# Kernel optimization log

Hardware: AMD Instinct MI355X
Metric: run time of the kernel (lower is better)

Reference implementation:

```python
import jax, jax.numpy as jnp
import numpy as np

B, S, E, H, DH, F = 4, 2048, 1024, 4, 256, 4096


def setup_inputs() -> dict:
    key = jax.random.key(0)
    ks = jax.random.split(key, 16)
    def w(k, shape):
        return jax.random.normal(k, shape, jnp.float32) * 0.02
    return {
        "inputs": jax.random.normal(ks[0], (B, S, E), jnp.float32),
        "context": jax.random.normal(ks[1], (B, S, E), jnp.float32),
        # self-attention (causal) per-head projections stacked over heads
        "Wk1": w(ks[2], (H, E, DH)), "bk1": jnp.zeros((H, DH), jnp.float32),
        "Wq1": w(ks[3], (H, E, DH)), "bq1": jnp.zeros((H, DH), jnp.float32),
        "Wv1": w(ks[4], (H, E, DH)), "bv1": jnp.zeros((H, DH), jnp.float32),
        "Wo1": w(ks[5], (E, E)), "bo1": jnp.zeros((E,), jnp.float32),
        # cross-attention (no mask)
        "Wk2": w(ks[6], (H, E, DH)), "bk2": jnp.zeros((H, DH), jnp.float32),
        "Wq2": w(ks[7], (H, E, DH)), "bq2": jnp.zeros((H, DH), jnp.float32),
        "Wv2": w(ks[8], (H, E, DH)), "bv2": jnp.zeros((H, DH), jnp.float32),
        "Wo2": w(ks[9], (E, E)), "bo2": jnp.zeros((E,), jnp.float32),
        "ln_g": jnp.ones((E,), jnp.float32), "ln_b": jnp.zeros((E,), jnp.float32),
        # FFN
        "W1": w(ks[10], (E, F)), "b1": jnp.zeros((F,), jnp.float32),
        "W2": w(ks[11], (F, E)), "b2": jnp.zeros((E,), jnp.float32),
    }


def _mha(kin, vin, qin, Wk, bk, Wq, bq, Wv, bv, Wo, bo, causal):
    # per-head Dense projections, batched over heads: [B,S,E] x [H,E,DH] -> [B,H,S,DH]
    K = jnp.einsum('bse,hed->bhsd', kin, Wk) + bk[None, :, None, :]
    Q = jnp.einsum('bse,hed->bhsd', qin, Wq) + bq[None, :, None, :]
    V = jnp.einsum('bse,hed->bhsd', vin, Wv) + bv[None, :, None, :]
    # NOTE: original divides by head_dim (K.get_shape()[2]), NOT sqrt(head_dim)
    scores = jnp.einsum('bhqd,bhkd->bhqk', Q, K) / K.shape[-1]
    if causal:
        sq, sk = scores.shape[-2], scores.shape[-1]
        mask = jnp.triu(jnp.full((sq, sk), -jnp.inf, scores.dtype), k=1)
        scores = scores + mask  # additive -inf strictly above the diagonal
    A = jax.nn.softmax(scores, axis=-1)
    # concat heads in order along the feature axis, then output Dense
    out = jnp.einsum('bhqk,bhkd->bqhd', A, V).reshape(qin.shape[0], qin.shape[1], -1)
    return out @ Wo + bo


def _ln(x, g, b):
    # keras LayerNormalization default epsilon = 1e-3
    m = x.mean(-1, keepdims=True)
    v = ((x - m) ** 2).mean(-1, keepdims=True)
    return (x - m) / jnp.sqrt(v + 1e-3) * g + b


def reference(inputs, context, Wk1, bk1, Wq1, bq1, Wv1, bv1, Wo1, bo1,
              Wk2, bk2, Wq2, bq2, Wv2, bv2, Wo2, bo2,
              ln_g, ln_b, W1, b1, W2, b2):
    # dropout layers are identity at inference
    a = _mha(inputs, inputs, inputs, Wk1, bk1, Wq1, bq1, Wv1, bv1, Wo1, bo1, True) + inputs
    a = _ln(a, ln_g, ln_b)
    # cross-attention: keys/values = context, queries = normalized self-attn output
    c = _mha(context, context, a, Wk2, bk2, Wq2, bq2, Wv2, bv2, Wo2, bo2, False) + a
    c = _ln(c, ln_g, ln_b)
    h = jax.nn.relu(c @ W1 + b1) @ W2 + b2 + c
    return jax.nn.relu(_ln(h, ln_g, ln_b))
```

## Files before the change

### kernel.cpp

```cpp
#include <hip/hip_runtime.h>

#define DEV __device__ __forceinline__

typedef unsigned short u16;
typedef __bf16 bf16x8 __attribute__((ext_vector_type(8)));
typedef bf16x8 __attribute__((may_alias)) bf16x8a;
typedef float f32x4 __attribute__((ext_vector_type(4)));
typedef float f32x16 __attribute__((ext_vector_type(16)));

constexpr int NB = 4, NS = 2048, NE = 1024, NH = 4, NDH = 256, NF = 4096;
constexpr int NR = NB * NS;

DEV u16 f2bf(float f) {
  unsigned u = __float_as_uint(f);
  u += 0x7fff + ((u >> 16) & 1);
  return (u16)(u >> 16);
}

DEV f32x4 mfma16(bf16x8 a, bf16x8 b, f32x4 c) {
  return __builtin_amdgcn_mfma_f32_16x16x32_bf16(a, b, c, 0, 0, 0);
}
DEV f32x16 mfma32(bf16x8 a, bf16x8 b, f32x16 c) {
  return __builtin_amdgcn_mfma_f32_32x32x16_bf16(a, b, c, 0, 0, 0);
}

DEV bf16x8 ldfrag(const u16* p) { return *(const bf16x8a*)p; }

DEV void gload_lds16(const void* g, void* l) {
  __builtin_amdgcn_global_load_lds(
      (const __attribute__((address_space(1))) void*)g,
      (__attribute__((address_space(3))) void*)l, 16, 0, 0);
}

DEV void blockbar() {
  asm volatile("" ::: "memory");
  __builtin_amdgcn_s_barrier();
  asm volatile("" ::: "memory");
}

DEV unsigned packbf(float a, float b) {
  union { __bf16 h[2]; unsigned u; } x;
  x.h[0] = (__bf16)a; x.h[1] = (__bf16)b;
  return x.u;
}

__global__ void cast_f32_bf16(const float* __restrict__ in, u16* __restrict__ out, int n4) {
  int i = blockIdx.x * 256 + threadIdx.x;
  if (i >= n4) return;
  float4 v = ((const float4*)in)[i];
  ushort4 o;
  o.x = f2bf(v.x); o.y = f2bf(v.y); o.z = f2bf(v.z); o.w = f2bf(v.w);
  ((ushort4*)out)[i] = o;
}

__global__ void transpose_cast(const float* __restrict__ in, u16* __restrict__ out, int R, int C) {
  __shared__ float t[32][33];
  size_t base = (size_t)blockIdx.z * R * C;
  int c0 = blockIdx.x * 32, r0 = blockIdx.y * 32;
  int x = threadIdx.x;
  for (int yy = threadIdx.y; yy < 32; yy += 8)
    t[yy][x] = in[base + (size_t)(r0 + yy) * C + c0 + x];
  __syncthreads();
  for (int yy = threadIdx.y; yy < 32; yy += 8)
    out[base + (size_t)(c0 + yy) * R + r0 + x] = f2bf(t[x][yy]);
}

__global__ void transpose_v(const u16* __restrict__ V, int vstride, u16* __restrict__ Vt) {
  __shared__ u16 t[32][34];
  int bh = blockIdx.z, b = bh >> 2, h = bh & (NH - 1);
  int s0 = blockIdx.x * 32, d0 = blockIdx.y * 32;
  int x = threadIdx.x;
  for (int yy = threadIdx.y; yy < 32; yy += 8)
    t[yy][x] = V[(size_t)(b * NS + s0 + yy) * vstride + h * NDH + d0 + x];
  __syncthreads();
  for (int yy = threadIdx.y; yy < 32; yy += 8)
    Vt[((size_t)bh * NDH + d0 + yy) * NS + s0 + x] = t[x][yy];
}

__global__ void copy_f32(const float* __restrict__ s, float* __restrict__ d, int n) {
  int i = blockIdx.x * 256 + threadIdx.x;
  if (i < n) d[i] = s[i];
}

template<int BN, int OUTF32, int RELU>
__global__ __launch_bounds__(512, 1)
void gemm8p(const u16* __restrict__ A, const u16* __restrict__ Bt,
            const float* __restrict__ bias, const float* __restrict__ res,
            float* __restrict__ outF, u16* __restrict__ outB,
            int M, int N, int K)
{
  constexpr int NFRAG = BN / 64;
  __shared__ __align__(16) u16 smem[32768 + 2 * BN * 64];

  int tid = threadIdx.x, w = tid >> 6, lane = tid & 63;
  int lr = lane & 15, lk = lane >> 4;
  int wm = w >> 2, wn = w & 3;

  int flat = blockIdx.y * gridDim.x + blockIdx.x;
  int cpx = (gridDim.x * gridDim.y) >> 3;
  int swz = (flat & 7) * cpx + (flat >> 3);
  int bx = swz % gridDim.x, by = swz / gridDim.x;
  int rowBlk = by * 256, colBlk = bx * BN;

  f32x4 acc[8][NFRAG];
#pragma unroll
  for (int f = 0; f < 8; f++)
#pragma unroll
    for (int n = 0; n < NFRAG; n++) acc[f][n] = (f32x4){0.f, 0.f, 0.f, 0.f};

  int srow = lane >> 3;
  int scol = ((lane & 7) ^ (srow & 7)) * 8;

  const u16* gA = A + (size_t)rowBlk * K;
  const u16* gB = Bt + (size_t)colBlk * K;

  auto stageA = [&](int t, int p, int h) {
#pragma unroll
    for (int j = 0; j < 2; j++) {
      int rbase = h * 128 + (w * 2 + j) * 8;
      gload_lds16(gA + (size_t)(rbase + srow) * K + t * 64 + scol,
                  &smem[(p * 256 + rbase) * 64]);
    }
  };
  auto stageB = [&](int t, int p, int h) {
#pragma unroll
    for (int j = 0; j < 2; j++) {
      int rbase = h * 128 + (w * 2 + j) * 8;
      gload_lds16(gB + (size_t)(rbase + srow) * K + t * 64 + scol,
                  &smem[32768 + (p * BN + rbase) * 64]);
    }
  };

  stageB(0, 0, 0);
  if (BN == 256) stageB(0, 0, 1);
  stageA(0, 0, 0);
  stageA(0, 0, 1);
  asm volatile("s_waitcnt vmcnt(0)" ::: "memory");
  blockbar();

  int NT = K >> 6;
  for (int t = 0; t < NT; t++) {
    int p = t & 1;
    bool pre = (t + 1 < NT);
    bf16x8 bf[NFRAG][2];
#pragma unroll
    for (int q = 0; q < 4; q++) {
      if (q == 0) {
#pragma unroll
        for (int n = 0; n < NFRAG; n++)
#pragma unroll
          for (int s = 0; s < 2; s++) {
            int rowB = wn * (BN >> 2) + n * 16 + lr;
            bf[n][s] = ldfrag(&smem[32768 + (p * BN + rowB) * 64 +
                                    (((s * 4 + lk) ^ (lr & 7)) * 8)]);
          }
      }
      bf16x8 af[2][2];
#pragma unroll
      for (int i = 0; i < 2; i++)
#pragma unroll
        for (int s = 0; s < 2; s++) {
          int rowA = wm * 128 + (q * 2 + i) * 16 + lr;
          af[i][s] = ldfrag(&smem[(p * 256 + rowA) * 64 +
                                  (((s * 4 + lk) ^ (lr & 7)) * 8)]);
        }
      if (pre) {
        if (BN == 256) {
          if (q == 0) { stageB(t + 1, p ^ 1, 0); stageB(t + 1, p ^ 1, 1); }
          else if (q == 1) stageA(t + 1, p ^ 1, 0);
          else if (q == 2) stageA(t + 1, p ^ 1, 1);
        } else {
          if (q == 0) stageB(t + 1, p ^ 1, 0);
          else if (q == 1) stageA(t + 1, p ^ 1, 0);
          else if (q == 2) stageA(t + 1, p ^ 1, 1);
        }
      }
      blockbar();
      asm volatile("s_waitcnt lgkmcnt(0)" ::: "memory");
      __builtin_amdgcn_s_setprio(1);
#pragma unroll
      for (int i = 0; i < 2; i++)
#pragma unroll
        for (int n = 0; n < NFRAG; n++)
#pragma unroll
          for (int s = 0; s < 2; s++)
            acc[q * 2 + i][n] = mfma16(af[i][s], bf[n][s], acc[q * 2 + i][n]);
      __builtin_amdgcn_s_setprio(0);
      if (q == 3) asm volatile("s_waitcnt vmcnt(0)" ::: "memory");
      blockbar();
    }
  }

  int orow0 = rowBlk + wm * 128;
  int ocol0 = colBlk + wn * (BN >> 2);
#pragma unroll
  for (int n = 0; n < NFRAG; n++) {
    int c = ocol0 + n * 16 + lr;
    float bv = bias[c];
#pragma unroll
    for (int f = 0; f < 8; f++) {
      int r0 = orow0 + f * 16 + lk * 4;
#pragma unroll
      for (int j = 0; j < 4; j++) {
        float v = acc[f][n][j] + bv;
        if (OUTF32) v += res[(size_t)(r0 + j) * N + c];
        if (RELU) v = fmaxf(v, 0.f);
        if (OUTF32) outF[(size_t)(r0 + j) * N + c] = v;
        else        outB[(size_t)(r0 + j) * N + c] = f2bf(v);
      }
    }
  }
}

template<int CAUSAL, int SPLIT>
__global__ __launch_bounds__(512, 2)
void attn8w(const u16* __restrict__ Qp, int qstride,
            const u16* __restrict__ Kp, int kstride,
            const u16* __restrict__ Vt, u16* __restrict__ O,
            float* __restrict__ Op, float* __restrict__ ml)
{
  __shared__ __align__(16) u16 smem[65536];

  int bidx = blockIdx.x;
  int bh, qt, kt0, kt1;
  if (SPLIT) {
    int qtIdx = bidx >> 5;
    qt = 15 - qtIdx;
    int sub = bidx & 31;
    int half = sub >> 4;
    bh = sub & 15;
    kt0 = half ? (qt + 1) : 0;
    kt1 = half ? (2 * qt + 2) : (qt + 1);
  } else {
    bh = bidx & 15;
    qt = CAUSAL ? (15 - (bidx >> 4)) : (bidx >> 4);
    kt0 = 0;
    kt1 = CAUSAL ? (2 * qt + 2) : (NS / 64);
  }
  int b = bh >> 2, h = bh & 3;
  int tid = threadIdx.x, w = tid >> 6, lane = tid & 63;
  int L = lane & 31, hi = lane >> 5;
  int g = w >> 1, ks = w & 1;

  int qbase = qt * 128 + g * 32;

  const u16* qrow = Qp + (size_t)(b * NS + qbase + L) * qstride + h * NDH;
  bf16x8 qf[16];
#pragma unroll
  for (int s = 0; s < 16; s++) qf[s] = ldfrag(qrow + s * 16 + hi * 8);

  f32x16 oacc[8];
#pragma unroll
  for (int db = 0; db < 8; db++) oacc[db] = (f32x16){};
  float m = -1e30f, l = 0.f;

  constexpr float SC = 1.0f / NDH;

  const u16* kbase = Kp + (size_t)(b * NS) * kstride + h * NDH;
  const u16* vbase = Vt + (size_t)bh * NDH * NS;

  auto stage = [&](int kt, int buf) {
#pragma unroll
    for (int ii = 0; ii < 4; ii++) {
      int gi = w * 4 + ii;
      int krow = 2 * gi + hi;
      int kcol = L ^ (krow & 31);
      gload_lds16(kbase + (size_t)(kt * 64 + krow) * kstride + kcol * 8,
                  &smem[buf * 16384 + gi * 512]);
      int vd = gi * 8 + (lane >> 3);
      int vg = (lane & 7) ^ (vd & 7);
      gload_lds16(vbase + (size_t)vd * NS + kt * 64 + vg * 8,
                  &smem[32768 + buf * 16384 + gi * 512]);
    }
  };

  stage(kt0, 0);
  asm volatile("" ::: "memory");

  for (int kt = kt0; kt < kt1; kt++) {
    int buf = (kt - kt0) & 1;
    const u16* bK = &smem[buf * 16384];
    const u16* bV = &smem[32768 + buf * 16384];
    if (kt + 1 < kt1) {
      stage(kt + 1, buf ^ 1);
      asm volatile("s_waitcnt vmcnt(8)" ::: "memory");
    } else {
      asm volatile("s_waitcnt vmcnt(0)" ::: "memory");
    }
    blockbar();

    int ksub0 = kt * 64 + ks * 32;
    bool skip = CAUSAL && (ksub0 > qbase + 31);
    if (!skip) {
      bool domask = CAUSAL && (ksub0 + 31 > qbase);
      __builtin_amdgcn_s_setprio(1);
      f32x16 sa = (f32x16){};
#pragma unroll
      for (int s = 0; s < 16; s++) {
        int row = ks * 32 + L;
        bf16x8 kf = ldfrag(&bK[row * 256 + (((2 * s + hi) ^ L) & 31) * 8]);
        sa = mfma32(kf, qf[s], sa);
      }
      __builtin_amdgcn_s_setprio(0);

      float p[16];
      float tmax = -1e30f;
#pragma unroll
      for (int r = 0; r < 16; r++) {
        float v = sa[r] * SC;
        if (domask) {
          int key = ksub0 + (r & 3) + 8 * (r >> 2) + 4 * hi;
          if (key > qbase + L) v = -1e30f;
        }
        p[r] = v;
        tmax = fmaxf(tmax, v);
      }
      tmax = fmaxf(tmax, __shfl_xor(tmax, 32));

      float mn = m;
      if (!__all(tmax - m <= 5.0f)) {
        mn = fmaxf(m, tmax);
        float rs = __expf(m - mn);
        m = mn;
        l *= rs;
#pragma unroll
        for (int db = 0; db < 8; db++)
#pragma unroll
          for (int r = 0; r < 16; r++) oacc[db][r] *= rs;
      }
      float psum = 0.f;
#pragma unroll
      for (int r = 0; r < 16; r++) {
        p[r] = __expf(p[r] - mn);
        psum += p[r];
      }
      psum += __shfl_xor(psum, 32);
      l += psum;

      unsigned pk01 = packbf(p[0], p[1]),  pk23 = packbf(p[2], p[3]);
      unsigned pk45 = packbf(p[4], p[5]),  pk67 = packbf(p[6], p[7]);
      unsigned pk89 = packbf(p[8], p[9]),  pkab = packbf(p[10], p[11]);
      unsigned pkcd = packbf(p[12], p[13]), pkef = packbf(p[14], p[15]);
      unsigned s45 = (unsigned)__shfl_xor((int)pk45, 32);
      unsigned s67 = (unsigned)__shfl_xor((int)pk67, 32);
      unsigned s01 = (unsigned)__shfl_xor((int)pk01, 32);
      unsigned s23 = (unsigned)__shfl_xor((int)pk23, 32);
      unsigned scd = (unsigned)__shfl_xor((int)pkcd, 32);
      unsigned sef = (unsigned)__shfl_xor((int)pkef, 32);
      unsigned s89 = (unsigned)__shfl_xor((int)pk89, 32);
      unsigned sab = (unsigned)__shfl_xor((int)pkab, 32);
      union { unsigned u[4]; bf16x8 v; } fb0, fb1;
      fb0.u[0] = hi ? s45 : pk01;
      fb0.u[1] = hi ? s67 : pk23;
      fb0.u[2] = hi ? pk45 : s01;
      fb0.u[3] = hi ? pk67 : s23;
      fb1.u[0] = hi ? scd : pk89;
      fb1.u[1] = hi ? sef : pkab;
      fb1.u[2] = hi ? pkcd : s89;
      fb1.u[3] = hi ? pkef : sab;
      bf16x8 pb0 = fb0.v, pb1 = fb1.v;

      __builtin_amdgcn_s_setprio(1);
#pragma unroll
      for (int db = 0; db < 8; db++) {
        int vd = db * 32 + L;
        bf16x8 vf0 = ldfrag(&bV[vd * 64 + (((ks * 4 + hi) ^ (vd & 7)) & 7) * 8]);
        bf16x8 vf1 = ldfrag(&bV[vd * 64 + (((ks * 4 + 2 + hi) ^ (vd & 7)) & 7) * 8]);
        oacc[db] = mfma32(vf0, pb0, oacc[db]);
        oacc[db] = mfma32(vf1, pb1, oacc[db]);
      }
      __builtin_amdgcn_s_setprio(0);
    }
    blockbar();
  }

  float* fsm = (float*)smem;
  blockbar();
  if (hi == 0) { fsm[w * 64 + L * 2] = m; fsm[w * 64 + L * 2 + 1] = l; }
  asm volatile("s_waitcnt lgkmcnt(0)" ::: "memory");
  blockbar();
  float mb = fsm[(w ^ 1) * 64 + L * 2];
  float lb = fsm[(w ^ 1) * 64 + L * 2 + 1];
  float M = fmaxf(m, mb);
  float eo = __expf(m - M);
  float lt = l * eo + lb * __expf(mb - M);
  asm volatile("s_waitcnt lgkmcnt(0)" ::: "memory");
  blockbar();
  float* reg = fsm + g * 8192;
  if (w & 1) {
#pragma unroll
    for (int db = 0; db < 8; db++)
#pragma unroll
      for (int r = 0; r < 16; r++) {
        int d = db * 32 + (r & 3) + 8 * (r >> 2) + 4 * hi;
        reg[d * 32 + L] = oacc[db][r] * eo;
      }
  }
  asm volatile("s_waitcnt lgkmcnt(0)" ::: "memory");
  blockbar();
  if (!(w & 1)) {
    if (SPLIT) {
      float* OpB = Op + (size_t)bidx * 32768 + (size_t)(g * 32 + L) * 256;
      if (hi == 0) {
        ml[((size_t)bidx * 128 + g * 32 + L) * 2]     = M;
        ml[((size_t)bidx * 128 + g * 32 + L) * 2 + 1] = lt;
      }
#pragma unroll
      for (int db = 0; db < 8; db++) {
#pragma unroll
        for (int rq = 0; rq < 4; rq++) {
          int d0 = db * 32 + rq * 8 + hi * 4;
          float4 v;
          v.x = oacc[db][rq * 4 + 0] * eo + reg[(d0 + 0) * 32 + L];
          v.y = oacc[db][rq * 4 + 1] * eo + reg[(d0 + 1) * 32 + L];
          v.z = oacc[db][rq * 4 + 2] * eo + reg[(d0 + 2) * 32 + L];
          v.w = oacc[db][rq * 4 + 3] * eo + reg[(d0 + 3) * 32 + L];
          *(float4*)(OpB + d0) = v;
        }
      }
    } else {
      float inv = 1.f / lt;
      size_t orow = (size_t)(b * NS + qbase + L) * NE + h * NDH;
#pragma unroll
      for (int db = 0; db < 8; db++) {
#pragma unroll
        for (int rq = 0; rq < 4; rq++) {
          int d0 = db * 32 + rq * 8 + hi * 4;
          float a0 = (oacc[db][rq * 4 + 0] * eo + reg[(d0 + 0) * 32 + L]) * inv;
          float a1 = (oacc[db][rq * 4 + 1] * eo + reg[(d0 + 1) * 32 + L]) * inv;
          float a2 = (oacc[db][rq * 4 + 2] * eo + reg[(d0 + 2) * 32 + L]) * inv;
          float a3 = (oacc[db][rq * 4 + 3] * eo + reg[(d0 + 3) * 32 + L]) * inv;
          uint2 wv;
          wv.x = packbf(a0, a1);
          wv.y = packbf(a2, a3);
          *(uint2*)&O[orow + d0] = wv;
        }
      }
    }
  }
}

__global__ __launch_bounds__(256)
void merge_attn(const float* __restrict__ Op, const float* __restrict__ ml,
                u16* __restrict__ O)
{
  int blk = blockIdx.x;
  int qt = blk >> 4, bh = blk & 15;
  int b = bh >> 2, h = bh & 3;
  int p0 = (15 - qt) * 32 + bh;
  int p1 = p0 + 16;
  int tid = threadIdx.x;
  int row = tid >> 1;
  int dbase = (tid & 1) * 128;

  float m0 = ml[((size_t)p0 * 128 + row) * 2];
  float l0 = ml[((size_t)p0 * 128 + row) * 2 + 1];
  float m1 = ml[((size_t)p1 * 128 + row) * 2];
  float l1 = ml[((size_t)p1 * 128 + row) * 2 + 1];
  float M = fmaxf(m0, m1);
  float e0 = __expf(m0 - M), e1 = __expf(m1 - M);
  float inv = 1.f / (l0 * e0 + l1 * e1);
  const float* O0 = Op + ((size_t)p0 * 128 + row) * 256 + dbase;
  const float* O1 = Op + ((size_t)p1 * 128 + row) * 256 + dbase;
  u16* dst = O + (size_t)(b * NS + qt * 128 + row) * NE + h * NDH + dbase;
#pragma unroll
  for (int d = 0; d < 128; d += 4) {
    float4 a = *(const float4*)(O0 + d);
    float4 c = *(const float4*)(O1 + d);
    uint2 wv;
    wv.x = packbf((a.x * e0 + c.x * e1) * inv, (a.y * e0 + c.y * e1) * inv);
    wv.y = packbf((a.z * e0 + c.z * e1) * inv, (a.w * e0 + c.w * e1) * inv);
    *(uint2*)(dst + d) = wv;
  }
}

template<int RELU, int WBF>
__global__ __launch_bounds__(256)
void ln_kernel(const float* __restrict__ x, const float* __restrict__ g,
               const float* __restrict__ bb, float* __restrict__ outF,
               u16* __restrict__ outB)
{
  int row = blockIdx.x, tid = threadIdx.x;
  float4 v = ((const float4*)(x + (size_t)row * NE))[tid];
  float s = v.x + v.y + v.z + v.w;
  float s2 = v.x * v.x + v.y * v.y + v.z * v.z + v.w * v.w;
#pragma unroll
  for (int off = 32; off; off >>= 1) {
    s += __shfl_xor(s, off);
    s2 += __shfl_xor(s2, off);
  }
  __shared__ float red[8];
  int wid = tid >> 6, lane = tid & 63;
  if (lane == 0) { red[wid] = s; red[4 + wid] = s2; }
  __syncthreads();
  s = red[0] + red[1] + red[2] + red[3];
  s2 = red[4] + red[5] + red[6] + red[7];
  float mean = s * (1.f / NE);
  float var = s2 * (1.f / NE) - mean * mean;
  float rstd = rsqrtf(var + 1e-3f);
  float4 gg = ((const float4*)g)[tid];
  float4 bv = ((const float4*)bb)[tid];
  float4 o;
  o.x = (v.x - mean) * rstd * gg.x + bv.x;
  o.y = (v.y - mean) * rstd * gg.y + bv.y;
  o.z = (v.z - mean) * rstd * gg.z + bv.z;
  o.w = (v.w - mean) * rstd * gg.w + bv.w;
  if (RELU) {
    o.x = fmaxf(o.x, 0.f); o.y = fmaxf(o.y, 0.f);
    o.z = fmaxf(o.z, 0.f); o.w = fmaxf(o.w, 0.f);
  }
  ((float4*)(outF + (size_t)row * NE))[tid] = o;
  if (WBF) {
    ushort4 ob;
    ob.x = f2bf(o.x); ob.y = f2bf(o.y); ob.z = f2bf(o.z); ob.w = f2bf(o.w);
    ((ushort4*)(outB + (size_t)row * NE))[tid] = ob;
  }
}

constexpr size_t OFF_X    = 0;
constexpr size_t OFF_W    = OFF_X + 16777216;
constexpr size_t OFF_BIAS = OFF_W + 33554432;
constexpr size_t OFF_QKV  = OFF_BIAS + 32768;
constexpr size_t OFF_VT   = OFF_QKV + 50331648;
constexpr size_t OFF_T0   = OFF_VT + 16777216;
constexpr size_t OFF_A    = OFF_T0 + 33554432;
constexpr size_t OFF_ABF  = OFF_A + 33554432;

extern "C" void kernel_launch(void* const* d_in, const int* in_sizes, int n_in,
                              void* d_out, int out_size, void* d_ws, size_t ws_size,
                              hipStream_t stream) {
  (void)in_sizes; (void)n_in; (void)out_size; (void)ws_size;
  const float* inp = (const float*)d_in[0];
  const float* ctx = (const float*)d_in[1];
  const float* Wk1 = (const float*)d_in[2];  const float* bk1 = (const float*)d_in[3];
  const float* Wq1 = (const float*)d_in[4];  const float* bq1 = (const float*)d_in[5];
  const float* Wv1 = (const float*)d_in[6];  const float* bv1 = (const float*)d_in[7];
  const float* Wo1 = (const float*)d_in[8];  const float* bo1 = (const float*)d_in[9];
  const float* Wk2 = (const float*)d_in[10]; const float* bk2 = (const float*)d_in[11];
  const float* Wq2 = (const float*)d_in[12]; const float* bq2 = (const float*)d_in[13];
  const float* Wv2 = (const float*)d_in[14]; const float* bv2 = (const float*)d_in[15];
  const float* Wo2 = (const float*)d_in[16]; const float* bo2 = (const float*)d_in[17];
  const float* lng = (const float*)d_in[18]; const float* lnb = (const float*)d_in[19];
  const float* W1  = (const float*)d_in[20]; const float* b1  = (const float*)d_in[21];
  const float* W2  = (const float*)d_in[22]; const float* b2  = (const float*)d_in[23];
  float* out = (float*)d_out;
  char* ws = (char*)d_ws;

  u16* XBF    = (u16*)(ws + OFF_X);
  u16* WQKV1T = (u16*)(ws + OFF_W);
  u16* WKV2T  = WQKV1T + 3072 * 1024;
  u16* WQ2T   = WKV2T + 2048 * 1024;
  u16* WO1T   = WQ2T + 1024 * 1024;
  u16* WO2T   = WO1T + 1024 * 1024;
  u16* W1T    = WO2T + 1024 * 1024;
  u16* W2T    = W1T + 4096 * 1024;
  float* BQKV1 = (float*)(ws + OFF_BIAS);
  float* BKV2  = BQKV1 + 3072;
  u16* QKV  = (u16*)(ws + OFF_QKV);
  u16* Q2   = QKV + 8192 * 2048;
  u16* VT   = (u16*)(ws + OFF_VT);
  u16* MID  = QKV;
  float* T0 = (float*)(ws + OFF_T0);
  float* OpBuf = T0;
  float* Af = (float*)(ws + OFF_A);
  u16* ABF  = (u16*)(ws + OFF_ABF);
  float* MlBuf = (float*)(ws + OFF_ABF);
  u16* Obuf = XBF;

  dim3 tb(32, 8);

  cast_f32_bf16<<<8192, 256, 0, stream>>>(inp, XBF, NR * NE / 4);
  transpose_cast<<<dim3(8, 32, 4), tb, 0, stream>>>(Wk1, WQKV1T,               NE, NDH);
  transpose_cast<<<dim3(8, 32, 4), tb, 0, stream>>>(Wq1, WQKV1T + 1024 * 1024, NE, NDH);
  transpose_cast<<<dim3(8, 32, 4), tb, 0, stream>>>(Wv1, WQKV1T + 2048 * 1024, NE, NDH);
  transpose_cast<<<dim3(32, 32, 1), tb, 0, stream>>>(Wo1, WO1T, NE, NE);
  transpose_cast<<<dim3(8, 32, 4), tb, 0, stream>>>(Wk2, WKV2T,               NE, NDH);
  transpose_cast<<<dim3(8, 32, 4), tb, 0, stream>>>(Wv2, WKV2T + 1024 * 1024, NE, NDH);
  transpose_cast<<<dim3(8, 32, 4), tb, 0, stream>>>(Wq2, WQ2T, NE, NDH);
  transpose_cast<<<dim3(32, 32, 1), tb, 0, stream>>>(Wo2, WO2T, NE, NE);
  transpose_cast<<<dim3(128, 32, 1), tb, 0, stream>>>(W1, W1T, NE, NF);
  transpose_cast<<<dim3(32, 128, 1), tb, 0, stream>>>(W2, W2T, NF, NE);
  copy_f32<<<4, 256, 0, stream>>>(bk1, BQKV1, 1024);
  copy_f32<<<4, 256, 0, stream>>>(bq1, BQKV1 + 1024, 1024);
  copy_f32<<<4, 256, 0, stream>>>(bv1, BQKV1 + 2048, 1024);
  copy_f32<<<4, 256, 0, stream>>>(bk2, BKV2, 1024);
  copy_f32<<<4, 256, 0, stream>>>(bv2, BKV2 + 1024, 1024);

  gemm8p<256, 0, 0><<<dim3(12, 32), 512, 0, stream>>>(XBF, WQKV1T, BQKV1, nullptr,
                                                      nullptr, QKV, NR, 3072, NE);
  transpose_v<<<dim3(64, 8, 16), tb, 0, stream>>>(QKV + 2048, 3072, VT);
  attn8w<1, 1><<<512, 512, 0, stream>>>(QKV + 1024, 3072, QKV, 3072, VT,
                                        nullptr, OpBuf, MlBuf);
  merge_attn<<<256, 256, 0, stream>>>(OpBuf, MlBuf, Obuf);
  gemm8p<128, 1, 0><<<dim3(8, 32), 512, 0, stream>>>(Obuf, WO1T, bo1, inp,
                                                     T0, nullptr, NR, NE, NE);
  ln_kernel<0, 1><<<NR, 256, 0, stream>>>(T0, lng, lnb, Af, ABF);

  cast_f32_bf16<<<8192, 256, 0, stream>>>(ctx, XBF, NR * NE / 4);
  gemm8p<256, 0, 0><<<dim3(8, 32), 512, 0, stream>>>(XBF, WKV2T, BKV2, nullptr,
                                                     nullptr, QKV, NR, 2048, NE);
  gemm8p<128, 0, 0><<<dim3(8, 32), 512, 0, stream>>>(ABF, WQ2T, bq2, nullptr,
                                                     nullptr, Q2, NR, NE, NE);
  transpose_v<<<dim3(64, 8, 16), tb, 0, stream>>>(QKV + 1024, 2048, VT);
  attn8w<0, 0><<<256, 512, 0, stream>>>(Q2, 1024, QKV, 2048, VT, Obuf,
                                        nullptr, nullptr);
  gemm8p<128, 1, 0><<<dim3(8, 32), 512, 0, stream>>>(Obuf, WO2T, bo2, Af,
                                                     T0, nullptr, NR, NE, NE);
  ln_kernel<0, 1><<<NR, 256, 0, stream>>>(T0, lng, lnb, Af, ABF);

  gemm8p<256, 0, 1><<<dim3(16, 32), 512, 0, stream>>>(ABF, W1T, b1, nullptr,
                                                      nullptr, MID, NR, NF, NE);
  gemm8p<128, 1, 0><<<dim3(8, 32), 512, 0, stream>>>(MID, W2T, b2, Af,
                                                     T0, nullptr, NR, NE, NF);
  ln_kernel<1, 0><<<NR, 256, 0, stream>>>(T0, lng, lnb, out, nullptr);
}
```

Measured before the change: 727.0 us.

## Replace 512-thread 256-row GEMM with 128x128 tile, 256-thread, two-blocks-per-CU GEMM

All dense projections and FFN GEMMs now use a new kernel with 128x128 output tiles, 4 waves and launch bounds allowing two blocks per CU, instead of a 256xBN tile with 8 waves at one block per CU. The K loop is simplified: the next tile is prefetched at the start of the iteration, all A/B fragments are loaded from LDS, all MFMAs are issued, and there is one barrier per iteration instead of four. The goal is more parallelism across the grid and less barrier overhead. The cost is lower per-block data reuse (more global/L2 traffic per FLOP) and more VGPRs per wave for fragments.

Measured after the change: 713.0 us. About the same (-1.9%).

```diff
diff --git a/kernel.cpp b/kernel.cpp
--- a/kernel.cpp
+++ b/kernel.cpp
@@ -82,124 +82,106 @@
   if (i < n) d[i] = s[i];
 }
 
-template<int BN, int OUTF32, int RELU>
-__global__ __launch_bounds__(512, 1)
-void gemm8p(const u16* __restrict__ A, const u16* __restrict__ Bt,
+template<int OUTF32, int RELU>
+__global__ __launch_bounds__(256, 2)
+void gemm2b(const u16* __restrict__ A, const u16* __restrict__ Bt,
             const float* __restrict__ bias, const float* __restrict__ res,
             float* __restrict__ outF, u16* __restrict__ outB,
             int M, int N, int K)
 {
-  constexpr int NFRAG = BN / 64;
-  __shared__ __align__(16) u16 smem[32768 + 2 * BN * 64];
+  __shared__ __align__(16) u16 smem[32768];
 
   int tid = threadIdx.x, w = tid >> 6, lane = tid & 63;
   int lr = lane & 15, lk = lane >> 4;
-  int wm = w >> 2, wn = w & 3;
 
   int flat = blockIdx.y * gridDim.x + blockIdx.x;
   int cpx = (gridDim.x * gridDim.y) >> 3;
   int swz = (flat & 7) * cpx + (flat >> 3);
   int bx = swz % gridDim.x, by = swz / gridDim.x;
-  int rowBlk = by * 256, colBlk = bx * BN;
-
-  f32x4 acc[8][NFRAG];
+  int rowBlk = by * 128, colBlk = bx * 128;
+
+  f32x4 acc[8][2];
 #pragma unroll
   for (int f = 0; f < 8; f++)
 #pragma unroll
-    for (int n = 0; n < NFRAG; n++) acc[f][n] = (f32x4){0.f, 0.f, 0.f, 0.f};
+    for (int n = 0; n < 2; n++) acc[f][n] = (f32x4){0.f, 0.f, 0.f, 0.f};
 
   int srow = lane >> 3;
-  int scol = ((lane & 7) ^ (srow & 7)) * 8;
+  int scol = ((lane & 7) ^ srow) * 8;
 
   const u16* gA = A + (size_t)rowBlk * K;
   const u16* gB = Bt + (size_t)colBlk * K;
 
-  auto stageA = [&](int t, int p, int h) {
-#pragma unroll
-    for (int j = 0; j < 2; j++) {
-      int rbase = h * 128 + (w * 2 + j) * 8;
-      gload_lds16(gA + (size_t)(rbase + srow) * K + t * 64 + scol,
-                  &smem[(p * 256 + rbase) * 64]);
+  auto stageA = [&](int t, int p) {
+#pragma unroll
+    for (int j = 0; j < 4; j++) {
+      int rbase = (w * 4 + j) * 8;
+      gload_lds16(gA + (size_t)(rbase + srow) * K + (size_t)t * 64 + scol,
+                  &smem[(p * 128 + rbase) * 64]);
     }
   };
-  auto stageB = [&](int t, int p, int h) {
-#pragma unroll
-    for (int j = 0; j < 2; j++) {
-      int rbase = h * 128 + (w * 2 + j) * 8;
-      gload_lds16(gB + (size_t)(rbase + srow) * K + t * 64 + scol,
-                  &smem[32768 + (p * BN + rbase) * 64]);
+  auto stageB = [&](int t, int p) {
+#pragma unroll
+    for (int j = 0; j < 4; j++) {
+      int rbase = (w * 4 + j) * 8;
+      gload_lds16(gB + (size_t)(rbase + srow) * K + (size_t)t * 64 + scol,
+                  &smem[16384 + (p * 128 + rbase) * 64]);
     }
   };
 
-  stageB(0, 0, 0);
-  if (BN == 256) stageB(0, 0, 1);
-  stageA(0, 0, 0);
-  stageA(0, 0, 1);
+  stageB(0, 0);
+  asm volatile("" ::: "memory");
+  stageA(0, 0);
   asm volatile("s_waitcnt vmcnt(0)" ::: "memory");
   blockbar();
 
   int NT = K >> 6;
   for (int t = 0; t < NT; t++) {
     int p = t & 1;
-    bool pre = (t + 1 < NT);
-    bf16x8 bf[NFRAG][2];
-#pragma unroll
-    for (int q = 0; q < 4; q++) {
-      if (q == 0) {
-#pragma unroll
-        for (int n = 0; n < NFRAG; n++)
-#pragma unroll
-          for (int s = 0; s < 2; s++) {
-            int rowB = wn * (BN >> 2) + n * 16 + lr;
-            bf[n][s] = ldfrag(&smem[32768 + (p * BN + rowB) * 64 +
-                                    (((s * 4 + lk) ^ (lr & 7)) * 8)]);
-          }
-      }
-      bf16x8 af[2][2];
-#pragma unroll
-      for (int i = 0; i < 2; i++)
-#pragma unroll
-        for (int s = 0; s < 2; s++) {
-          int rowA = wm * 128 + (q * 2 + i) * 16 + lr;
-          af[i][s] = ldfrag(&smem[(p * 256 + rowA) * 64 +
-                                  (((s * 4 + lk) ^ (lr & 7)) * 8)]);
-        }
-      if (pre) {
-        if (BN == 256) {
-          if (q == 0) { stageB(t + 1, p ^ 1, 0); stageB(t + 1, p ^ 1, 1); }
-          else if (q == 1) stageA(t + 1, p ^ 1, 0);
-          else if (q == 2) stageA(t + 1, p ^ 1, 1);
-        } else {
-          if (q == 0) stageB(t + 1, p ^ 1, 0);
-          else if (q == 1) stageA(t + 1, p ^ 1, 0);
-          else if (q == 2) stageA(t + 1, p ^ 1, 1);
-        }
-      }
-      blockbar();
-      asm volatile("s_waitcnt lgkmcnt(0)" ::: "memory");
-      __builtin_amdgcn_s_setprio(1);
-#pragma unroll
-      for (int i = 0; i < 2; i++)
-#pragma unroll
-        for (int n = 0; n < NFRAG; n++)
-#pragma unroll
-          for (int s = 0; s < 2; s++)
-            acc[q * 2 + i][n] = mfma16(af[i][s], bf[n][s], acc[q * 2 + i][n]);
-      __builtin_amdgcn_s_setprio(0);
-      if (q == 3) asm volatile("s_waitcnt vmcnt(0)" ::: "memory");
-      blockbar();
-    }
-  }
-
-  int orow0 = rowBlk + wm * 128;
-  int ocol0 = colBlk + wn * (BN >> 2);
-#pragma unroll
-  for (int n = 0; n < NFRAG; n++) {
+    if (t + 1 < NT) {
+      stageB(t + 1, p ^ 1);
+      asm volatile("" ::: "memory");
+      stageA(t + 1, p ^ 1);
+      asm volatile("" ::: "memory");
+    }
+    const u16* Ar = &smem[p * 8192];
+    const u16* Br = &smem[16384 + p * 8192];
+    bf16x8 bf[2][2], af[8][2];
+#pragma unroll
+    for (int n = 0; n < 2; n++)
+#pragma unroll
+      for (int s = 0; s < 2; s++) {
+        int rowB = w * 32 + n * 16 + lr;
+        bf[n][s] = ldfrag(&Br[rowB * 64 + (((s * 4 + lk) ^ (lr & 7)) * 8)]);
+      }
+#pragma unroll
+    for (int f = 0; f < 8; f++)
+#pragma unroll
+      for (int s = 0; s < 2; s++) {
+        int rowA = f * 16 + lr;
+        af[f][s] = ldfrag(&Ar[rowA * 64 + (((s * 4 + lk) ^ (lr & 7)) * 8)]);
+      }
+    __builtin_amdgcn_s_setprio(1);
+#pragma unroll
+    for (int f = 0; f < 8; f++)
+#pragma unroll
+      for (int n = 0; n < 2; n++)
+#pragma unroll
+        for (int s = 0; s < 2; s++)
+          acc[f][n] = mfma16(af[f][s], bf[n][s], acc[f][n]);
+    __builtin_amdgcn_s_setprio(0);
+    asm volatile("s_waitcnt vmcnt(0)" ::: "memory");
+    blockbar();
+  }
+
+  int ocol0 = colBlk + w * 32;
+#pragma unroll
+  for (int n = 0; n < 2; n++) {
     int c = ocol0 + n * 16 + lr;
     float bv = bias[c];
 #pragma unroll
     for (int f = 0; f < 8; f++) {
-      int r0 = orow0 + f * 16 + lk * 4;
+      int r0 = rowBlk + f * 16 + lk * 4;
 #pragma unroll
       for (int j = 0; j < 4; j++) {
         float v = acc[f][n][j] + bv;
@@ -586,31 +568,31 @@
   copy_f32<<<4, 256, 0, stream>>>(bk2, BKV2, 1024);
   copy_f32<<<4, 256, 0, stream>>>(bv2, BKV2 + 1024, 1024);
 
-  gemm8p<256, 0, 0><<<dim3(12, 32), 512, 0, stream>>>(XBF, WQKV1T, BQKV1, nullptr,
-                                                      nullptr, QKV, NR, 3072, NE);
+  gemm2b<0, 0><<<dim3(24, 64), 256, 0, stream>>>(XBF, WQKV1T, BQKV1, nullptr,
+                                                 nullptr, QKV, NR, 3072, NE);
   transpose_v<<<dim3(64, 8, 16), tb, 0, stream>>>(QKV + 2048, 3072, VT);
   attn8w<1, 1><<<512, 512, 0, stream>>>(QKV + 1024, 3072, QKV, 3072, VT,
                                         nullptr, OpBuf, MlBuf);
   merge_attn<<<256, 256, 0, stream>>>(OpBuf, MlBuf, Obuf);
-  gemm8p<128, 1, 0><<<dim3(8, 32), 512, 0, stream>>>(Obuf, WO1T, bo1, inp,
-                                                     T0, nullptr, NR, NE, NE);
+  gemm2b<1, 0><<<dim3(8, 64), 256, 0, stream>>>(Obuf, WO1T, bo1, inp,
+                                                T0, nullptr, NR, NE, NE);
   ln_kernel<0, 1><<<NR, 256, 0, stream>>>(T0, lng, lnb, Af, ABF);
 
   cast_f32_bf16<<<8192, 256, 0, stream>>>(ctx, XBF, NR * NE / 4);
-  gemm8p<256, 0, 0><<<dim3(8, 32), 512, 0, stream>>>(XBF, WKV2T, BKV2, nullptr,
-                                                     nullptr, QKV, NR, 2048, NE);
-  gemm8p<128, 0, 0><<<dim3(8, 32), 512, 0, stream>>>(ABF, WQ2T, bq2, nullptr,
-                                                     nullptr, Q2, NR, NE, NE);
+  gemm2b<0, 0><<<dim3(16, 64), 256, 0, stream>>>(XBF, WKV2T, BKV2, nullptr,
+                                                 nullptr, QKV, NR, 2048, NE);
+  gemm2b<0, 0><<<dim3(8, 64), 256, 0, stream>>>(ABF, WQ2T, bq2, nullptr,
+                                                nullptr, Q2, NR, NE, NE);
   transpose_v<<<dim3(64, 8, 16), tb, 0, stream>>>(QKV + 1024, 2048, VT);
   attn8w<0, 0><<<256, 512, 0, stream>>>(Q2, 1024, QKV, 2048, VT, Obuf,
                                         nullptr, nullptr);
-  gemm8p<128, 1, 0><<<dim3(8, 32), 512, 0, stream>>>(Obuf, WO2T, bo2, Af,
-                                                     T0, nullptr, NR, NE, NE);
+  gemm2b<1, 0><<<dim3(8, 64), 256, 0, stream>>>(Obuf, WO2T, bo2, Af,
+                                                T0, nullptr, NR, NE, NE);
   ln_kernel<0, 1><<<NR, 256, 0, stream>>>(T0, lng, lnb, Af, ABF);
 
-  gemm8p<256, 0, 1><<<dim3(16, 32), 512, 0, stream>>>(ABF, W1T, b1, nullptr,
-                                                      nullptr, MID, NR, NF, NE);
-  gemm8p<128, 1, 0><<<dim3(8, 32), 512, 0, stream>>>(MID, W2T, b2, Af,
-                                                     T0, nullptr, NR, NE, NF);
+  gemm2b<0, 1><<<dim3(32, 64), 256, 0, stream>>>(ABF, W1T, b1, nullptr,
+                                                 nullptr, MID, NR, NF, NE);
+  gemm2b<1, 0><<<dim3(8, 64), 256, 0, stream>>>(MID, W2T, b2, Af,
+                                                T0, nullptr, NR, NE, NF);
   ln_kernel<1, 0><<<NR, 256, 0, stream>>>(T0, lng, lnb, out, nullptr);
 }
```
